# Optimization experiments

Measured on AMD Instinct MI355X. Metric: run time of the kernel, lower is better.

## Reference

```python
import jax, jax.numpy as jnp
import numpy as np

H = 8            # heads
M = 256          # num_landmarks
PINV_ITERS = 6
PAD = 16         # residual_conv_kernel(33)//2


def layernorm(x, g, b, eps=1e-5):
    mu = x.mean(-1, keepdims=True)
    var = ((x - mu) ** 2).mean(-1, keepdims=True)
    return (x - mu) * jax.lax.rsqrt(var + eps) * g + b


def moore_penrose_pinv(x, iters=PINV_ITERS):
    # iterative Moore-Penrose pseudo-inverse (Nystromformer)
    abs_x = jnp.abs(x)
    col = abs_x.sum(-1)
    row = abs_x.sum(-2)
    z = jnp.swapaxes(x, -1, -2) / (jnp.max(col) * jnp.max(row))
    eye = jnp.eye(x.shape[-1], dtype=x.dtype)
    for _ in range(iters):
        xz = x @ z
        z = 0.25 * z @ (13.0 * eye - xz @ (15.0 * eye - xz @ (7.0 * eye - xz)))
    return z


def attn_block(y, ln1_g, ln1_b, w_qkv, w_out, b_out, res_w,
               ln2_g, ln2_b, w1, b1, w2, b2):
    B, N, D = y.shape
    inner = w_qkv.shape[1] // 3
    dh = inner // H
    xn = layernorm(y, ln1_g, ln1_b)
    qkv = xn @ w_qkv                      # [B,N,3*inner]
    q, k, v = jnp.split(qkv, 3, axis=-1)
    to_heads = lambda t: t.reshape(B, N, H, dh).transpose(0, 2, 1, 3)  # [B,H,N,dh]
    q, k, v = map(to_heads, (q, k, v))
    q = q * (dh ** -0.5)
    l = N // M                            # tokens per landmark (N % M == 0 here)
    q_l = q.reshape(B, H, M, l, dh).mean(3)  # sum/l == mean -> [B,H,M,dh]
    k_l = k.reshape(B, H, M, l, dh).mean(3)
    attn1 = jax.nn.softmax(jnp.einsum('bhnd,bhmd->bhnm', q, k_l), axis=-1)
    attn2 = jax.nn.softmax(jnp.einsum('bhid,bhjd->bhij', q_l, k_l), axis=-1)
    attn3 = jax.nn.softmax(jnp.einsum('bhmd,bhnd->bhmn', q_l, k), axis=-1)
    attn2_inv = moore_penrose_pinv(attn2)
    out = (attn1 @ attn2_inv) @ (attn3 @ v)   # [B,H,N,dh]
    # depthwise residual conv over sequence dim: v as NCHW with C=H, Hdim=N, Wdim=dh
    res = jax.lax.conv_general_dilated(
        v, res_w, window_strides=(1, 1), padding=[(PAD, PAD), (0, 0)],
        dimension_numbers=('NCHW', 'OIHW', 'NCHW'), feature_group_count=H)
    out = out + res
    out = out.transpose(0, 2, 1, 3).reshape(B, N, inner)
    y = y + out @ w_out + b_out
    yn = layernorm(y, ln2_g, ln2_b)
    hdn = jax.nn.gelu(yn @ w1 + b1, approximate=False)
    return y + hdn @ w2 + b2


def setup_inputs() -> dict:
    key = jax.random.key(0)
    ks = jax.random.split(key, 8)
    B, N, D, NB = 4, 4096, 256, 2
    inner = D
    p = lambda k, shp: jax.random.normal(k, shp, jnp.float32) * 0.02
    return {
        'x': jax.random.normal(ks[0], (B, N, D), jnp.float32),
        'ln1_g': jnp.ones((NB, D), jnp.float32),
        'ln1_b': jnp.zeros((NB, D), jnp.float32),
        'w_qkv': p(ks[1], (NB, D, 3 * inner)),
        'w_out': p(ks[2], (NB, inner, D)),
        'b_out': jnp.zeros((NB, D), jnp.float32),
        'res_w': p(ks[3], (NB, H, 1, 33, 1)),
        'ln2_g': jnp.ones((NB, D), jnp.float32),
        'ln2_b': jnp.zeros((NB, D), jnp.float32),
        'w1': p(ks[4], (NB, D, 2 * D)),
        'b1': jnp.zeros((NB, 2 * D), jnp.float32),
        'w2': p(ks[5], (NB, 2 * D, D)),
        'b2': jnp.zeros((NB, D), jnp.float32),
    }


def reference(x, ln1_g, ln1_b, w_qkv, w_out, b_out, res_w,
              ln2_g, ln2_b, w1, b1, w2, b2):
    y = x
    for i in range(ln1_g.shape[0]):
        y = attn_block(y, ln1_g[i], ln1_b[i], w_qkv[i], w_out[i], b_out[i],
                       res_w[i], ln2_g[i], ln2_b[i], w1[i], b1[i], w2[i], b2[i])
    return y
```

## Files before the change

### kernel.cpp

```cpp
#include <hip/hip_runtime.h>
#include <math.h>

typedef float f32x4 __attribute__((ext_vector_type(4)));
typedef short s16x8 __attribute__((ext_vector_type(8)));
typedef unsigned short u16;
typedef unsigned int u32;

#define MFMA16(a,b,c) __builtin_amdgcn_mfma_f32_16x16x32_bf16((a),(b),(c),0,0,0)
#define AS1 __attribute__((address_space(1)))
#define AS3 __attribute__((address_space(3)))

__device__ __forceinline__ void dma16(const u16* g, u16* l){
  __builtin_amdgcn_global_load_lds((const AS1 u32*)g, (AS3 u32*)l, 16, 0, 0);
}

__device__ __forceinline__ float bf2f(u16 u){
  union { unsigned int i; float f; } v; v.i = ((unsigned int)u)<<16; return v.f;
}
__device__ __forceinline__ u16 f2bf(float f){
  union { float f; unsigned int i; } v; v.f = f;
  unsigned int x = v.i;
  return (u16)((x + 0x7fffu + ((x>>16)&1u))>>16);
}

enum { EPI_QKV=0, EPI_BIAS_GELU=3 };

template<int EPI>
__global__ __launch_bounds__(256)
void kgemm2(const u16* __restrict__ A, const u16* __restrict__ BT, int K, int lda, int ldb,
            const float* __restrict__ bias, u16* __restrict__ outb, int ldc,
            u16* __restrict__ qo, u16* __restrict__ ko, u16* __restrict__ vo,
            u16* __restrict__ qlm, u16* __restrict__ klm)
{
  __shared__ __align__(16) u16 As[128*32];
  __shared__ __align__(16) u16 Bs[128*32];
  const int tid = threadIdx.x;
  const int w = tid>>6, wy = w>>1, wx = w&1, l = tid&63, q = l>>4, ln = l&15;
  const int m0 = blockIdx.x*128, n0 = blockIdx.y*128;
  const int lrow = l>>2, lch = l&3;

  f32x4 acc[4][4];
  #pragma unroll
  for (int i=0;i<4;i++)
    #pragma unroll
    for (int j=0;j<4;j++){ acc[i][j][0]=0.f; acc[i][j][1]=0.f; acc[i][j][2]=0.f; acc[i][j][3]=0.f; }

  for (int k0=0; k0<K; k0+=32){
    #pragma unroll
    for (int c=0;c<2;c++){
      int row = 32*w + 16*c + lrow;
      int gch = lch ^ ((row>>1)&3);
      dma16(A + (long)(m0+row)*lda + k0 + gch*8, &As[(32*w+16*c)*32]);
      dma16(BT + (long)(n0+row)*ldb + k0 + gch*8, &Bs[(32*w+16*c)*32]);
    }
    __syncthreads();
    s16x8 af[4], bfr[4];
    #pragma unroll
    for (int mt=0;mt<4;mt++){
      int row = wy*64 + mt*16 + ln;
      af[mt] = *(const s16x8*)&As[row*32 + ((q ^ ((row>>1)&3))<<3)];
    }
    #pragma unroll
    for (int nt=0;nt<4;nt++){
      int row = wx*64 + nt*16 + ln;
      bfr[nt] = *(const s16x8*)&Bs[row*32 + ((q ^ ((row>>1)&3))<<3)];
    }
    #pragma unroll
    for (int mt=0;mt<4;mt++)
      #pragma unroll
      for (int nt=0;nt<4;nt++)
        acc[mt][nt] = MFMA16(af[mt], bfr[nt], acc[mt][nt]);
    __syncthreads();
  }

  #pragma unroll
  for (int mt=0;mt<4;mt++)
  #pragma unroll
  for (int nt=0;nt<4;nt++){
    int ncol = n0 + wx*64 + nt*16 + ln;
    if (EPI==EPI_QKV){
      int sel = ncol>>8, hd = ncol&255, h = hd>>5, d = hd&31;
      u16* dst = sel==0 ? qo : (sel==1 ? ko : vo);
      float sc2 = (sel==0) ? 0.17677669529663689f : 1.f;
      float s = 0.f;
      #pragma unroll
      for (int r=0;r<4;r++){
        int mrow = m0 + wy*64 + mt*16 + q*4 + r;
        int b = mrow>>12, n = mrow&4095;
        float v = acc[mt][nt][r]*sc2;
        dst[(((long)(b*8+h)*4096 + n)<<5) + d] = f2bf(v);
        s += v;
      }
      if (sel < 2){
        s += __shfl_xor(s, 16);
        s += __shfl_xor(s, 32);
        if (q == 0){
          int mrow0 = m0 + wy*64 + mt*16;
          int b = mrow0>>12, grp = (mrow0&4095)>>4;
          u16* ldst = (sel==0) ? qlm : klm;
          ldst[(((long)(b*8+h)*256 + grp)<<5) + d] = f2bf(s*(1.0f/16.0f));
        }
      }
    } else {
      #pragma unroll
      for (int r=0;r<4;r++){
        int mrow = m0 + wy*64 + mt*16 + q*4 + r;
        float x = acc[mt][nt][r] + bias[ncol];
        float g = 0.5f*x*(1.0f + erff(x*0.70710678118654752f));
        outb[(long)mrow*ldc + ncol] = f2bf(g);
      }
    }
  }
}

__global__ __launch_bounds__(256)
void kgemmLN(const u16* __restrict__ A, const u16* __restrict__ BT, int K,
             const float* __restrict__ bias, const float* __restrict__ base,
             float* __restrict__ yout,
             const float* __restrict__ lng, const float* __restrict__ lnb,
             u16* __restrict__ xnout)
{
  __shared__ __align__(16) u16 As[128*32];
  __shared__ __align__(16) u16 Bs[256*32];
  const int tid = threadIdx.x;
  const int w = tid>>6, l = tid&63, q = l>>4, ln = l&15;
  const int m0 = blockIdx.x*128;
  const int lrow = l>>2, lch = l&3;

  f32x4 acc[2][16];
  #pragma unroll
  for (int i=0;i<2;i++)
    #pragma unroll
    for (int j=0;j<16;j++){ acc[i][j][0]=0.f; acc[i][j][1]=0.f; acc[i][j][2]=0.f; acc[i][j][3]=0.f; }

  for (int k0=0; k0<K; k0+=32){
    #pragma unroll
    for (int c=0;c<2;c++){
      int row = 32*w + 16*c + lrow;
      int gch = lch ^ ((row>>1)&3);
      dma16(A + (long)(m0+row)*K + k0 + gch*8, &As[(32*w+16*c)*32]);
    }
    #pragma unroll
    for (int c=0;c<4;c++){
      int row = 64*w + 16*c + lrow;
      int gch = lch ^ ((row>>1)&3);
      dma16(BT + (long)row*K + k0 + gch*8, &Bs[(64*w+16*c)*32]);
    }
    __syncthreads();
    s16x8 af[2];
    #pragma unroll
    for (int mt=0;mt<2;mt++){
      int row = w*32 + mt*16 + ln;
      af[mt] = *(const s16x8*)&As[row*32 + ((q ^ ((row>>1)&3))<<3)];
    }
    #pragma unroll
    for (int nt=0;nt<16;nt++){
      int row = nt*16 + ln;
      s16x8 bfr = *(const s16x8*)&Bs[row*32 + ((q ^ ((row>>1)&3))<<3)];
      acc[0][nt] = MFMA16(af[0], bfr, acc[0][nt]);
      acc[1][nt] = MFMA16(af[1], bfr, acc[1][nt]);
    }
    __syncthreads();
  }

  float rb[16];
  #pragma unroll
  for (int nt=0;nt<16;nt++) rb[nt] = bias[nt*16 + ln];
  #pragma unroll
  for (int mt=0;mt<2;mt++)
  #pragma unroll
  for (int r=0;r<4;r++){
    long rowb = (long)(m0 + w*32 + mt*16 + q*4 + r)*256;
    #pragma unroll
    for (int nt=0;nt<16;nt++){
      int col = nt*16 + ln;
      float v = base[rowb + col] + acc[mt][nt][r] + rb[nt];
      acc[mt][nt][r] = v;
      yout[rowb + col] = v;
    }
  }
  float mu[2][4], rs[2][4];
  #pragma unroll
  for (int mt=0;mt<2;mt++)
  #pragma unroll
  for (int r=0;r<4;r++){
    float s = 0.f;
    #pragma unroll
    for (int nt=0;nt<16;nt++) s += acc[mt][nt][r];
    s += __shfl_xor(s,1); s += __shfl_xor(s,2); s += __shfl_xor(s,4); s += __shfl_xor(s,8);
    mu[mt][r] = s*(1.0f/256.0f);
  }
  #pragma unroll
  for (int mt=0;mt<2;mt++)
  #pragma unroll
  for (int r=0;r<4;r++){
    float vs = 0.f;
    #pragma unroll
    for (int nt=0;nt<16;nt++){ float d = acc[mt][nt][r]-mu[mt][r]; vs += d*d; }
    vs += __shfl_xor(vs,1); vs += __shfl_xor(vs,2); vs += __shfl_xor(vs,4); vs += __shfl_xor(vs,8);
    rs[mt][r] = rsqrtf(vs*(1.0f/256.0f) + 1e-5f);
  }
  float rg[16], rbb[16];
  #pragma unroll
  for (int nt=0;nt<16;nt++){ int col = nt*16+ln; rg[nt]=lng[col]; rbb[nt]=lnb[col]; }
  #pragma unroll
  for (int mt=0;mt<2;mt++)
  #pragma unroll
  for (int r=0;r<4;r++){
    long rowb = (long)(m0 + w*32 + mt*16 + q*4 + r)*256;
    #pragma unroll
    for (int nt=0;nt<16;nt++){
      int col = nt*16 + ln;
      float d = acc[mt][nt][r]-mu[mt][r];
      xnout[rowb + col] = f2bf(d*rs[mt][r]*rg[nt] + rbb[nt]);
    }
  }
}

__device__ __forceinline__ int swidx(int row, int col){
  int cc = col>>3;
  int sl = (cc&24)|((cc&7)^((row>>1)&7));
  return row*256 + sl*8 + (col&7);
}

__device__ __forceinline__ void stage256(const u16* __restrict__ g, u16* lds, int w, int l){
  const int drow = l>>5, dch = l&31;
  #pragma unroll
  for (int c=0;c<16;c++){
    int base = (c*8 + w)*2;
    int row = base + drow;
    int gch = (dch&24) | ((dch&7) ^ ((row>>1)&7));
    dma16(g + (long)row*256 + gch*8, &lds[base*256]);
  }
}

__device__ __forceinline__ void stage32(const u16* __restrict__ g, u16* lds, int w, int l){
  const int drow = l>>5, dch = l&31;
  #pragma unroll
  for (int c=0;c<2;c++){
    int base = (c*8 + w)*2;
    int row = base + drow;
    int gch = (dch&24) | ((dch&7) ^ ((row>>1)&7));
    dma16(g + (long)row*256 + gch*8, &lds[base*256]);
  }
}

__device__ __forceinline__ void mult32(const u16* aL, int arow0, const u16* bL,
                                       int w, int l, f32x4 (&acc)[2][2]){
  const int q=l>>4, ln=l&15, wn0=w*32;
  #pragma unroll
  for (int mt=0;mt<2;mt++)
    #pragma unroll
    for (int nt=0;nt<2;nt++){ acc[mt][nt][0]=0.f; acc[mt][nt][1]=0.f; acc[mt][nt][2]=0.f; acc[mt][nt][3]=0.f; }
  #pragma unroll
  for (int kq=0;kq<8;kq++){
    int ca = kq*4+q;
    s16x8 af[2];
    #pragma unroll
    for (int mt=0;mt<2;mt++){
      int r = arow0 + mt*16 + ln;
      af[mt] = *(const s16x8*)&aL[r*256 + (((ca&24)|((ca&7)^((r>>1)&7)))<<3)];
    }
    #pragma unroll
    for (int nt=0;nt<2;nt++){
      int n = wn0 + nt*16 + ln;
      s16x8 bfr = *(const s16x8*)&bL[n*256 + (((ca&24)|((ca&7)^((n>>1)&7)))<<3)];
      acc[0][nt] = MFMA16(af[0], bfr, acc[0][nt]);
      acc[1][nt] = MFMA16(af[1], bfr, acc[1][nt]);
    }
  }
}

__device__ __forceinline__ void polyinit13(const u16* aL, int arow0, int w, int l, f32x4 (&poly)[2][2]){
  const int q=l>>4, ln=l&15, wn0=w*32;
  #pragma unroll
  for (int mt=0;mt<2;mt++)
  #pragma unroll
  for (int nt=0;nt<2;nt++)
  #pragma unroll
  for (int r=0;r<4;r++){
    int row = arow0 + mt*16 + q*4 + r;
    int col = wn0 + nt*16 + ln;
    poly[mt][nt][r] = 13.f*bf2f(aL[swidx(row,col)]);
  }
}

__device__ __forceinline__ void polyaxpy(f32x4 (&poly)[2][2], const f32x4 (&acc)[2][2], float sc){
  #pragma unroll
  for (int mt=0;mt<2;mt++)
    #pragma unroll
    for (int nt=0;nt<2;nt++)
      #pragma unroll
      for (int r=0;r<4;r++) poly[mt][nt][r] += sc*acc[mt][nt][r];
}

__device__ __forceinline__ void writeT(u16* Ts, const f32x4 (&acc)[2][2], int w, int l, float sc){
  const int q=l>>4, ln=l&15, wn0=w*32;
  #pragma unroll
  for (int mt=0;mt<2;mt++)
  #pragma unroll
  for (int nt=0;nt<2;nt++)
  #pragma unroll
  for (int r=0;r<4;r++){
    int row = mt*16 + q*4 + r;
    int col = wn0 + nt*16 + ln;
    Ts[swidx(row,col)] = f2bf(sc*acc[mt][nt][r]);
  }
}

__device__ __forceinline__ void epi_poly(u16* __restrict__ out, int rowbase,
                                         const f32x4 (&poly)[2][2], int w, int l, float sc){
  const int q=l>>4, ln=l&15, wn0=w*32;
  #pragma unroll
  for (int mt=0;mt<2;mt++)
  #pragma unroll
  for (int nt=0;nt<2;nt++)
  #pragma unroll
  for (int r=0;r<4;r++){
    int row = rowbase + mt*16 + q*4 + r;
    int col = wn0 + nt*16 + ln;
    out[(long)row*256 + col] = f2bf(sc*poly[mt][nt][r]);
  }
}

__global__ __launch_bounds__(512)
void kw0(const float* __restrict__ cs_p, float* __restrict__ scal,
         const float* __restrict__ num_p, const float* __restrict__ den_p,
         const u16* __restrict__ X, u16* __restrict__ W0, u16* __restrict__ h0)
{
  __shared__ __align__(16) u16 Wf[65536];
  __shared__ __align__(16) u16 Ts[8192];
  const int tid=threadIdx.x, w=tid>>6, l=tid&63;
  const int bid=blockIdx.x, xcd=bid&7, j=bid>>3;
  const int batch = xcd*4 + (j>>3), slab = j&7;

  stage256(X + (long)batch*65536, Wf, w, l);

  float* red = (float*)Ts;
  float mx = 0.f;
  for (int i=tid;i<8192;i+=512){
    float s = 0.f;
    #pragma unroll
    for (int c=0;c<8;c++) s += cs_p[(long)c*8192 + i];
    mx = fmaxf(mx, s);
  }
  red[tid] = mx; __syncthreads();
  for (int s=256;s>0;s>>=1){ if (tid<s) red[tid] = fmaxf(red[tid], red[tid+s]); __syncthreads(); }
  float s0 = 1.0f/red[0];
  if (bid==0 && tid==0) scal[0] = s0;

  f32x4 acc[2][2];
  mult32(Wf, slab*32, Wf, w, l, acc);
  {
    const int q=l>>4, ln=l&15, wn0=w*32;
    u16* ob = W0 + (long)batch*65536;
    #pragma unroll
    for (int mt=0;mt<2;mt++)
    #pragma unroll
    for (int nt=0;nt<2;nt++)
    #pragma unroll
    for (int r=0;r<4;r++){
      int row = slab*32 + mt*16 + q*4 + r;
      int col = wn0 + nt*16 + ln;
      ob[(long)row*256 + col] = f2bf(acc[mt][nt][r]*s0);
    }
  }

  if (slab==0){
    __syncthreads();
    float (*lt)[257] = (float(*)[257])Wf;
    for (int i=tid;i<8192;i+=512){
      int m = i>>5, d = i&31;
      float sn = 0.f, sd = 0.f;
      #pragma unroll
      for (int c=0;c<8;c++){
        sn += num_p[((long)(c*32+batch))*8192 + i];
        sd += den_p[(c*32+batch)*256 + m];
      }
      lt[d][m] = sn/sd;
    }
    __syncthreads();
    u16* o = h0 + (long)batch*8192;
    for (int j2=tid;j2<8192;j2+=512){
      int d = j2>>8, m = j2&255;
      o[j2] = f2bf(lt[d][m]);
    }
  }
}

__global__ __launch_bounds__(512)
void kiter(const u16* __restrict__ Win, u16* __restrict__ Wout,
           const u16* __restrict__ hin, u16* __restrict__ hout)
{
  __shared__ __align__(16) u16 Wf[65536];
  __shared__ __align__(16) u16 Ts[8192];
  const int tid=threadIdx.x, w=tid>>6, l=tid&63;
  const int bid=blockIdx.x, xcd=bid&7, j=bid>>3;
  const int batch = xcd*4 + (j>>3), slab = j&7;

  stage256(Win + (long)batch*65536, Wf, w, l);
  __syncthreads();

  f32x4 acc[2][2], poly[2][2];
  polyinit13(Wf, slab*32, w, l, poly);
  mult32(Wf, slab*32, Wf, w, l, acc);
  polyaxpy(poly, acc, -15.f);
  writeT(Ts, acc, w, l, 1.f);
  __syncthreads();
  mult32(Ts, 0, Wf, w, l, acc);
  polyaxpy(poly, acc, 7.f);
  __syncthreads();
  writeT(Ts, acc, w, l, 1.f);
  __syncthreads();
  mult32(Ts, 0, Wf, w, l, acc);
  polyaxpy(poly, acc, -1.f);
  epi_poly(Wout + (long)batch*65536, slab*32, poly, w, l, 0.25f);

  if (slab==0){
    __syncthreads();
    stage32(hin + (long)batch*8192, Ts, w, l);
    __syncthreads();
    polyinit13(Ts, 0, w, l, poly);
    mult32(Ts, 0, Wf, w, l, acc);
    polyaxpy(poly, acc, -15.f);
    __syncthreads(); writeT(Ts, acc, w, l, 1.f); __syncthreads();
    mult32(Ts, 0, Wf, w, l, acc);
    polyaxpy(poly, acc, 7.f);
    __syncthreads(); writeT(Ts, acc, w, l, 1.f); __syncthreads();
    mult32(Ts, 0, Wf, w, l, acc);
    polyaxpy(poly, acc, -1.f);
    epi_poly(hout + (long)batch*8192, 0, poly, w, l, 0.25f);
  }
}

__global__ __launch_bounds__(512)
void ktail(const u16* __restrict__ W5, const u16* __restrict__ h5,
           const u16* __restrict__ XT, const float* __restrict__ scal,
           u16* __restrict__ uT)
{
  __shared__ __align__(16) u16 Wf[65536];
  __shared__ __align__(16) u16 Ts[8192];
  const int tid=threadIdx.x, w=tid>>6, l=tid&63;
  const int batch = blockIdx.x;

  stage256(W5 + (long)batch*65536, Wf, w, l);
  stage32(h5 + (long)batch*8192, Ts, w, l);
  __syncthreads();

  f32x4 acc[2][2], poly[2][2];
  polyinit13(Ts, 0, w, l, poly);
  mult32(Ts, 0, Wf, w, l, acc);
  polyaxpy(poly, acc, -15.f);
  __syncthreads(); writeT(Ts, acc, w, l, 1.f); __syncthreads();
  mult32(Ts, 0, Wf, w, l, acc);
  polyaxpy(poly, acc, 7.f);
  __syncthreads(); writeT(Ts, acc, w, l, 1.f); __syncthreads();
  mult32(Ts, 0, Wf, w, l, acc);
  polyaxpy(poly, acc, -1.f);
  __syncthreads();
  writeT(Ts, poly, w, l, 0.25f);
  __syncthreads();
  stage256(XT + (long)batch*65536, Wf, w, l);
  __syncthreads();
  mult32(Ts, 0, Wf, w, l, acc);
  const float s0 = scal[0];
  {
    const int q=l>>4, ln=l&15, wn0=w*32;
    u16* ob = uT + (long)batch*8192;
    #pragma unroll
    for (int mt=0;mt<2;mt++)
    #pragma unroll
    for (int nt=0;nt<2;nt++)
    #pragma unroll
    for (int r=0;r<4;r++){
      int row = mt*16 + q*4 + r;
      int col = wn0 + nt*16 + ln;
      ob[(long)row*256 + col] = f2bf(acc[mt][nt][r]*s0);
    }
  }
}

__global__ __launch_bounds__(256)
void kattn23(const u16* __restrict__ ql, const u16* __restrict__ kl,
             u16* __restrict__ X, u16* __restrict__ XT, float* __restrict__ cs_p,
             const u16* __restrict__ kk, const u16* __restrict__ vv,
             float* __restrict__ num_p, float* __restrict__ den_p)
{
  __shared__ __align__(16) u16 Pbuf[4][64][40];
  __shared__ __align__(16) u16 vT[32][40];
  __shared__ float qrow[32][33];
  __shared__ float psum[32][4];
  __shared__ float rsum[32];
  int bh = blockIdx.y;
  int tid = threadIdx.x, w = tid>>6, l = tid&63, q = l>>4, ln = l&15;

  if (blockIdx.x < 8){
    int r0 = blockIdx.x*32;
    int c = tid;
    #pragma unroll
    for (int i=0;i<4;i++){
      int e = c*4+i; int rr = e>>5, dd = e&31;
      qrow[rr][dd] = bf2f(ql[((long)bh*256 + r0+rr)*32 + dd]);
    }
    float kc[32];
    {
      const u16* kp = kl + ((long)bh*256 + c)*32;
      #pragma unroll
      for (int d=0;d<32;d++) kc[d] = bf2f(kp[d]);
    }
    __syncthreads();
    float er[32]; float colacc = 0.f;
    for (int r=0;r<32;r++){
      float s = 0.f;
      #pragma unroll
      for (int d=0;d<32;d++) s += qrow[r][d]*kc[d];
      float e = __expf(s);
      er[r] = e;
      float wsum = e;
      #pragma unroll
      for (int m=1;m<64;m<<=1) wsum += __shfl_xor(wsum, m);
      if (l==0) psum[r][w] = wsum;
    }
    __syncthreads();
    if (c<32) rsum[c] = psum[c][0]+psum[c][1]+psum[c][2]+psum[c][3];
    __syncthreads();
    for (int r=0;r<32;r++){
      float x = er[r]/rsum[r];
      u16 xb = f2bf(x);
      X [((long)bh*256 + r0+r)*256 + c] = xb;
      XT[((long)bh*256 + c)*256 + r0+r] = xb;
      colacc += x;
    }
    cs_p[(long)blockIdx.x*8192 + bh*256 + c] = colacc;
    return;
  }

  int chunk = blockIdx.x - 8;
  f32x4 z4; z4[0]=0.f; z4[1]=0.f; z4[2]=0.f; z4[3]=0.f;
  f32x4 acc[4][2]; f32x4 dacc[4];
  #pragma unroll
  for (int mt=0;mt<4;mt++){ dacc[mt]=z4; acc[mt][0]=z4; acc[mt][1]=z4; }
  const u16* qlb = ql + (long)bh*8192;
  const u16* kb  = kk + (long)bh*131072;
  const u16* vb  = vv + (long)bh*131072;
  int vn = tid>>3, vd = (tid&7)*4;
  for (int s=0;s<16;s++){
    int n0 = chunk*512 + s*32;
    ushort4 vx = *(const ushort4*)(vb + (long)(n0+vn)*32 + vd);
    vT[vd+0][vn]=vx.x; vT[vd+1][vn]=vx.y; vT[vd+2][vn]=vx.z; vT[vd+3][vn]=vx.w;
    __syncthreads();
    s16x8 bk[2];
    #pragma unroll
    for (int nt=0;nt<2;nt++) bk[nt] = *(const s16x8*)(kb + (long)(n0 + nt*16 + ln)*32 + q*8);
    #pragma unroll
    for (int mt=0;mt<4;mt++){
      s16x8 aq = *(const s16x8*)(qlb + (long)(w*64 + mt*16 + ln)*32 + q*8);
      #pragma unroll
      for (int nt=0;nt<2;nt++){
        f32x4 sf = MFMA16(aq, bk[nt], z4);
        f32x4 ef;
        #pragma unroll
        for (int r=0;r<4;r++) ef[r] = __expf(sf[r]);
        dacc[mt] += ef;
        #pragma unroll
        for (int r=0;r<4;r++) Pbuf[w][mt*16 + q*4 + r][nt*16 + ln] = f2bf(ef[r]);
      }
    }
    #pragma unroll
    for (int mt=0;mt<4;mt++){
      s16x8 ap = *(const s16x8*)&Pbuf[w][mt*16 + ln][q*8];
      #pragma unroll
      for (int nt=0;nt<2;nt++){
        s16x8 bv = *(const s16x8*)&vT[nt*16 + ln][q*8];
        acc[mt][nt] = MFMA16(ap, bv, acc[mt][nt]);
      }
    }
    __syncthreads();
  }
  #pragma unroll
  for (int mt=0;mt<4;mt++)
    #pragma unroll
    for (int r=0;r<4;r++){
      float x = dacc[mt][r];
      x += __shfl_xor(x,1); x += __shfl_xor(x,2); x += __shfl_xor(x,4); x += __shfl_xor(x,8);
      dacc[mt][r] = x;
    }
  long pbase = (long)(chunk*32 + bh);
  #pragma unroll
  for (int mt=0;mt<4;mt++)
    #pragma unroll
    for (int nt=0;nt<2;nt++)
      #pragma unroll
      for (int r=0;r<4;r++){
        int mg = w*64 + mt*16 + q*4 + r;
        num_p[pbase*8192 + (long)mg*32 + nt*16 + ln] = acc[mt][nt][r];
      }
  if (ln==0){
    #pragma unroll
    for (int mt=0;mt<4;mt++)
      #pragma unroll
      for (int r=0;r<4;r++)
        den_p[pbase*256 + w*64 + mt*16 + q*4 + r] = dacc[mt][r];
  }
}

__global__ __launch_bounds__(256)
void kattn1u(const u16* __restrict__ qq, const u16* __restrict__ kl, const u16* __restrict__ uT,
             const u16* __restrict__ vv, const float* __restrict__ rw,
             u16* __restrict__ aoutb)
{
  int nch = blockIdx.x, bh = blockIdx.y;
  int b = bh>>3, h = bh&7;
  int tid = threadIdx.x, w = tid>>6, l = tid&63, q = l>>4, ln = l&15;
  __shared__ __align__(16) u16 Pbuf[4][32][40];
  __shared__ __align__(16) u16 vtile[160][36];
  int r0g = nch*128;
  const u16* vb = vv + (long)bh*131072;
  #pragma unroll
  for (int it=0; it<5; it++){
    int slot = tid + it*256;
    int rr = slot>>3, c = (slot&7)*4;
    int s = r0g - 16 + rr;
    ushort4 val; val.x=0; val.y=0; val.z=0; val.w=0;
    if (s>=0 && s<4096) val = *(const ushort4*)(vb + (long)s*32 + c);
    *(ushort4*)&vtile[rr][c] = val;
  }
  __syncthreads();

  f32x4 z4; z4[0]=0.f; z4[1]=0.f; z4[2]=0.f; z4[3]=0.f;
  f32x4 acc[2][2]; f32x4 dacc[2];
  #pragma unroll
  for (int mt=0;mt<2;mt++){ dacc[mt]=z4; acc[mt][0]=z4; acc[mt][1]=z4; }
  const u16* qb  = qq + (long)bh*131072;
  const u16* klb = kl + (long)bh*8192;
  const u16* ub  = uT + (long)bh*8192;
  int r0 = r0g + w*32;
  for (int s=0;s<8;s++){
    s16x8 bk[2];
    #pragma unroll
    for (int nt=0;nt<2;nt++) bk[nt] = *(const s16x8*)(klb + (long)(s*32 + nt*16 + ln)*32 + q*8);
    #pragma unroll
    for (int mt=0;mt<2;mt++){
      s16x8 aq = *(const s16x8*)(qb + (long)(r0 + mt*16 + ln)*32 + q*8);
      #pragma unroll
      for (int nt=0;nt<2;nt++){
        f32x4 sf = MFMA16(aq, bk[nt], z4);
        f32x4 ef;
        #pragma unroll
        for (int r=0;r<4;r++) ef[r] = __expf(sf[r]);
        dacc[mt] += ef;
        #pragma unroll
        for (int r=0;r<4;r++) Pbuf[w][mt*16 + q*4 + r][nt*16 + ln] = f2bf(ef[r]);
      }
    }
    #pragma unroll
    for (int mt=0;mt<2;mt++){
      s16x8 ap = *(const s16x8*)&Pbuf[w][mt*16 + ln][q*8];
      #pragma unroll
      for (int nt=0;nt<2;nt++){
        s16x8 bu = *(const s16x8*)(ub + (long)(nt*16 + ln)*256 + s*32 + q*8);
        acc[mt][nt] = MFMA16(ap, bu, acc[mt][nt]);
      }
    }
  }
  #pragma unroll
  for (int mt=0;mt<2;mt++)
    #pragma unroll
    for (int r=0;r<4;r++){
      float x = dacc[mt][r];
      x += __shfl_xor(x,1); x += __shfl_xor(x,2); x += __shfl_xor(x,4); x += __shfl_xor(x,8);
      dacc[mt][r] = x;
    }

  const float* wp = rw + h*33;
  float w_[33];
  #pragma unroll
  for (int j=0;j<33;j++) w_[j] = wp[j];

  #pragma unroll
  for (int mt=0;mt<2;mt++){
    int nl = w*32 + mt*16 + q*4;
    #pragma unroll
    for (int nt=0;nt<2;nt++){
      int d = nt*16 + ln;
      float vvv[36];
      #pragma unroll
      for (int j=0;j<36;j++) vvv[j] = bf2f(vtile[nl + j][d]);
      #pragma unroll
      for (int r=0;r<4;r++){
        float cv = 0.f;
        #pragma unroll
        for (int j=0;j<33;j++) cv += w_[j]*vvv[r+j];
        int n = r0 + mt*16 + q*4 + r;
        long oidx = ((long)b*4096 + n)*256 + h*32 + d;
        aoutb[oidx] = f2bf(acc[mt][nt][r]/dacc[mt][r] + cv);
      }
    }
  }
}

__global__ __launch_bounds__(256)
void kcvtln(const float* __restrict__ xin, const float* __restrict__ lg, const float* __restrict__ lb,
            u16* __restrict__ xn,
            const float* __restrict__ wqkv, const float* __restrict__ wout,
            const float* __restrict__ w1, const float* __restrict__ w2,
            u16* __restrict__ wqkvT, u16* __restrict__ woutT,
            u16* __restrict__ w1T, u16* __restrict__ w2T)
{
  __shared__ float t[32][33];
  int z = blockIdx.x;
  if (z < 4096){
    int w = threadIdx.x>>6, l = threadIdx.x&63;
    long row = (long)z*4 + w;
    float4 v = ((const float4*)(xin + row*256))[l];
    float s = v.x+v.y+v.z+v.w;
    #pragma unroll
    for (int m=1;m<64;m<<=1) s += __shfl_xor(s, m);
    float mu = s*(1.0f/256.0f);
    float dx=v.x-mu, dy=v.y-mu, dz=v.z-mu, dw=v.w-mu;
    float s2 = dx*dx+dy*dy+dz*dz+dw*dw;
    #pragma unroll
    for (int m=1;m<64;m<<=1) s2 += __shfl_xor(s2, m);
    float rs = rsqrtf(s2*(1.0f/256.0f) + 1e-5f);
    float4 gg = ((const float4*)lg)[l];
    float4 bb = ((const float4*)lb)[l];
    ushort4 o;
    o.x = f2bf(dx*rs*gg.x + bb.x);
    o.y = f2bf(dy*rs*gg.y + bb.y);
    o.z = f2bf(dz*rs*gg.z + bb.z);
    o.w = f2bf(dw*rs*gg.w + bb.w);
    *(ushort4*)(xn + row*256 + l*4) = o;
    return;
  }
  z -= 4096;
  const float* src; u16* dst; int K, Nn, bx, by;
  if (z < 384){      int i=z/192, r=z%192; src=wqkv+(long)i*196608; dst=wqkvT+(long)i*196608; K=256; Nn=768; bx=r%24; by=r/24; }
  else if (z < 512){ int zz=z-384; int i=zz/64, r=zz%64; src=wout+(long)i*65536; dst=woutT+(long)i*65536; K=256; Nn=256; bx=r%8; by=r/8; }
  else if (z < 768){ int zz=z-512; int i=zz/128, r=zz%128; src=w1+(long)i*131072; dst=w1T+(long)i*131072; K=256; Nn=512; bx=r%16; by=r/16; }
  else {             int zz=z-768; int i=zz/128, r=zz%128; src=w2+(long)i*131072; dst=w2T+(long)i*131072; K=512; Nn=256; bx=r%8; by=r/8; }
  int n0 = bx*32, k0 = by*32;
  int tx = threadIdx.x&31, ty = threadIdx.x>>5;
  #pragma unroll
  for (int i=0;i<4;i++) t[ty+i*8][tx] = src[(long)(k0+ty+i*8)*Nn + n0+tx];
  __syncthreads();
  #pragma unroll
  for (int i=0;i<4;i++) dst[(long)(n0+ty+i*8)*K + k0+tx] = f2bf(t[tx][ty+i*8]);
}

extern "C" void kernel_launch(void* const* d_in, const int* in_sizes, int n_in,
                              void* d_out, int out_size, void* d_ws, size_t ws_size,
                              hipStream_t stream)
{
  const float* x    = (const float*)d_in[0];
  const float* ln1g = (const float*)d_in[1];
  const float* ln1b = (const float*)d_in[2];
  const float* wqkv = (const float*)d_in[3];
  const float* wout = (const float*)d_in[4];
  const float* bout = (const float*)d_in[5];
  const float* resw = (const float*)d_in[6];
  const float* ln2g = (const float*)d_in[7];
  const float* ln2b = (const float*)d_in[8];
  const float* w1   = (const float*)d_in[9];
  const float* b1   = (const float*)d_in[10];
  const float* w2   = (const float*)d_in[11];
  const float* b2   = (const float*)d_in[12];
  float* y = (float*)d_out;
  char* ws = (char*)d_ws;

  u16* xn    = (u16*)(ws + 0);
  u16* qb    = (u16*)(ws + 8388608);
  u16* kb    = (u16*)(ws + 16777216);
  u16* vb    = (u16*)(ws + 25165824);
  u16* ql    = (u16*)(ws + 33554432);
  u16* kl    = (u16*)(ws + 34078720);
  u16* X     = (u16*)(ws + 34603008);
  u16* XT    = (u16*)(ws + 38797312);
  u16* h0b   = (u16*)(ws + 42991616);
  u16* WA    = (u16*)(ws + 51380224);
  u16* WB    = (u16*)(ws + 55574528);
  u16* hA    = (u16*)(ws + 68157440);
  u16* hB    = (u16*)(ws + 72351744);
  float* num_p = (float*)(ws + 76546048);
  float* den_p = (float*)(ws + 84934656);
  float* cs_p  = (float*)(ws + 85196800);
  float* scal  = (float*)(ws + 85458944);
  u16* uT    = (u16*)(ws + 85459200);
  u16* aoutb = (u16*)(ws + 85983488);
  u16* wqkvT = (u16*)(ws + 94372096);
  u16* woutT = (u16*)(ws + 95158528);
  u16* w1T   = (u16*)(ws + 95420672);
  u16* w2T   = (u16*)(ws + 95944960);
  u16* hdn   = (u16*)(ws + 51380224);

  (void)in_sizes; (void)n_in; (void)out_size; (void)ws_size;

  kcvtln<<<5120,256,0,stream>>>(x, ln1g, ln1b, xn,
      wqkv, wout, w1, w2, wqkvT, woutT, w1T, w2T);

  for (int i=0;i<2;i++){
    kgemm2<EPI_QKV><<<dim3(128,6),256,0,stream>>>(xn, wqkvT + (long)i*196608, 256, 256, 256,
        nullptr, nullptr, 0, qb,kb,vb, ql,kl);
    kattn23<<<dim3(16,32),256,0,stream>>>(ql, kl, X, XT, cs_p, kb, vb, num_p, den_p);

    kw0<<<256,512,0,stream>>>(cs_p, scal, num_p, den_p, X, WA, h0b);
    u16 *Wi = WA, *Wo = WB, *hi = h0b, *ho = hA;
    for (int it=0; it<5; it++){
      kiter<<<256,512,0,stream>>>(Wi, Wo, hi, ho);
      u16* t = Wi; Wi = Wo; Wo = t;
      hi = ho; ho = (ho == hA) ? hB : hA;
    }
    ktail<<<32,512,0,stream>>>(Wi, hi, XT, scal, uT);

    kattn1u<<<dim3(32,32),256,0,stream>>>(qb, kl, uT, vb, resw + i*264, aoutb);
    kgemmLN<<<128,256,0,stream>>>(aoutb, woutT + (long)i*65536, 256,
        bout + i*256, i==0 ? x : y, y, ln2g + i*256, ln2b + i*256, xn);
    kgemm2<EPI_BIAS_GELU><<<dim3(128,4),256,0,stream>>>(xn, w1T + (long)i*131072, 256, 256, 256,
        b1 + i*512, hdn, 512, nullptr,nullptr,nullptr, nullptr,nullptr);
    kgemmLN<<<128,256,0,stream>>>(hdn, w2T + (long)i*131072, 512,
        b2 + i*256, y, y, ln1g + 256, ln1b + 256, xn);
  }
}
```

Before: 536.7 us.

## Spread h-iteration across slabs, cache B fragments in registers, shrink LN-GEMM tiles

```diff
diff --git a/kernel.cpp b/kernel.cpp
--- a/kernel.cpp
+++ b/kernel.cpp
@@ -120,99 +120,111 @@
              const float* __restrict__ lng, const float* __restrict__ lnb,
              u16* __restrict__ xnout)
 {
-  __shared__ __align__(16) u16 As[128*32];
+  __shared__ __align__(16) u16 As[64*32];
   __shared__ __align__(16) u16 Bs[256*32];
+  __shared__ float red[64][4];
   const int tid = threadIdx.x;
   const int w = tid>>6, l = tid&63, q = l>>4, ln = l&15;
-  const int m0 = blockIdx.x*128;
-  const int lrow = l>>2, lch = l&3;
-
-  f32x4 acc[2][16];
-  #pragma unroll
-  for (int i=0;i<2;i++)
-    #pragma unroll
-    for (int j=0;j<16;j++){ acc[i][j][0]=0.f; acc[i][j][1]=0.f; acc[i][j][2]=0.f; acc[i][j][3]=0.f; }
+  const int m0 = blockIdx.x*64;
+
+  f32x4 acc[4][4];
+  #pragma unroll
+  for (int i=0;i<4;i++)
+    #pragma unroll
+    for (int j=0;j<4;j++){ acc[i][j][0]=0.f; acc[i][j][1]=0.f; acc[i][j][2]=0.f; acc[i][j][3]=0.f; }
 
   for (int k0=0; k0<K; k0+=32){
-    #pragma unroll
-    for (int c=0;c<2;c++){
-      int row = 32*w + 16*c + lrow;
-      int gch = lch ^ ((row>>1)&3);
-      dma16(A + (long)(m0+row)*K + k0 + gch*8, &As[(32*w+16*c)*32]);
+    {
+      int row = w*16 + (l>>2);
+      int gch = (l&3) ^ ((row>>1)&3);
+      dma16(A + (long)(m0+row)*K + k0 + gch*8, &As[(w*16)*32]);
     }
     #pragma unroll
     for (int c=0;c<4;c++){
-      int row = 64*w + 16*c + lrow;
-      int gch = lch ^ ((row>>1)&3);
-      dma16(BT + (long)row*K + k0 + gch*8, &Bs[(64*w+16*c)*32]);
-    }
-    __syncthreads();
-    s16x8 af[2];
-    #pragma unroll
-    for (int mt=0;mt<2;mt++){
-      int row = w*32 + mt*16 + ln;
+      int row = c*64 + w*16 + (l>>2);
+      int gch = (l&3) ^ ((row>>1)&3);
+      dma16(BT + (long)row*K + k0 + gch*8, &Bs[(c*64+w*16)*32]);
+    }
+    __syncthreads();
+    s16x8 af[4], bfr[4];
+    #pragma unroll
+    for (int mt=0;mt<4;mt++){
+      int row = mt*16 + ln;
       af[mt] = *(const s16x8*)&As[row*32 + ((q ^ ((row>>1)&3))<<3)];
     }
     #pragma unroll
-    for (int nt=0;nt<16;nt++){
-      int row = nt*16 + ln;
-      s16x8 bfr = *(const s16x8*)&Bs[row*32 + ((q ^ ((row>>1)&3))<<3)];
-      acc[0][nt] = MFMA16(af[0], bfr, acc[0][nt]);
-      acc[1][nt] = MFMA16(af[1], bfr, acc[1][nt]);
-    }
-    __syncthreads();
-  }
-
-  float rb[16];
-  #pragma unroll
-  for (int nt=0;nt<16;nt++) rb[nt] = bias[nt*16 + ln];
-  #pragma unroll
-  for (int mt=0;mt<2;mt++)
+    for (int nt=0;nt<4;nt++){
+      int row = w*64 + nt*16 + ln;
+      bfr[nt] = *(const s16x8*)&Bs[row*32 + ((q ^ ((row>>1)&3))<<3)];
+    }
+    #pragma unroll
+    for (int mt=0;mt<4;mt++)
+      #pragma unroll
+      for (int nt=0;nt<4;nt++)
+        acc[mt][nt] = MFMA16(af[mt], bfr[nt], acc[mt][nt]);
+    __syncthreads();
+  }
+
+  float rb[4];
+  #pragma unroll
+  for (int nt=0;nt<4;nt++) rb[nt] = bias[w*64 + nt*16 + ln];
+  #pragma unroll
+  for (int mt=0;mt<4;mt++)
   #pragma unroll
   for (int r=0;r<4;r++){
-    long rowb = (long)(m0 + w*32 + mt*16 + q*4 + r)*256;
-    #pragma unroll
-    for (int nt=0;nt<16;nt++){
-      int col = nt*16 + ln;
+    long rowb = (long)(m0 + mt*16 + q*4 + r)*256;
+    #pragma unroll
+    for (int nt=0;nt<4;nt++){
+      int col = w*64 + nt*16 + ln;
       float v = base[rowb + col] + acc[mt][nt][r] + rb[nt];
       acc[mt][nt][r] = v;
       yout[rowb + col] = v;
     }
   }
-  float mu[2][4], rs[2][4];
-  #pragma unroll
-  for (int mt=0;mt<2;mt++)
+  #pragma unroll
+  for (int mt=0;mt<4;mt++)
   #pragma unroll
   for (int r=0;r<4;r++){
-    float s = 0.f;
-    #pragma unroll
-    for (int nt=0;nt<16;nt++) s += acc[mt][nt][r];
+    float s = acc[mt][0][r]+acc[mt][1][r]+acc[mt][2][r]+acc[mt][3][r];
     s += __shfl_xor(s,1); s += __shfl_xor(s,2); s += __shfl_xor(s,4); s += __shfl_xor(s,8);
-    mu[mt][r] = s*(1.0f/256.0f);
-  }
-  #pragma unroll
-  for (int mt=0;mt<2;mt++)
+    if (ln==0) red[mt*16+q*4+r][w] = s;
+  }
+  __syncthreads();
+  float mu[4][4];
+  #pragma unroll
+  for (int mt=0;mt<4;mt++)
+  #pragma unroll
+  for (int r=0;r<4;r++){
+    int row = mt*16+q*4+r;
+    mu[mt][r] = (red[row][0]+red[row][1]+red[row][2]+red[row][3])*(1.0f/256.0f);
+  }
+  __syncthreads();
+  #pragma unroll
+  for (int mt=0;mt<4;mt++)
   #pragma unroll
   for (int r=0;r<4;r++){
     float vs = 0.f;
     #pragma unroll
-    for (int nt=0;nt<16;nt++){ float d = acc[mt][nt][r]-mu[mt][r]; vs += d*d; }
+    for (int nt=0;nt<4;nt++){ float d = acc[mt][nt][r]-mu[mt][r]; vs += d*d; }
     vs += __shfl_xor(vs,1); vs += __shfl_xor(vs,2); vs += __shfl_xor(vs,4); vs += __shfl_xor(vs,8);
-    rs[mt][r] = rsqrtf(vs*(1.0f/256.0f) + 1e-5f);
-  }
-  float rg[16], rbb[16];
-  #pragma unroll
-  for (int nt=0;nt<16;nt++){ int col = nt*16+ln; rg[nt]=lng[col]; rbb[nt]=lnb[col]; }
-  #pragma unroll
-  for (int mt=0;mt<2;mt++)
+    if (ln==0) red[mt*16+q*4+r][w] = vs;
+  }
+  __syncthreads();
+  float rg[4], rbb[4];
+  #pragma unroll
+  for (int nt=0;nt<4;nt++){ int col = w*64+nt*16+ln; rg[nt]=lng[col]; rbb[nt]=lnb[col]; }
+  #pragma unroll
+  for (int mt=0;mt<4;mt++)
   #pragma unroll
   for (int r=0;r<4;r++){
-    long rowb = (long)(m0 + w*32 + mt*16 + q*4 + r)*256;
-    #pragma unroll
-    for (int nt=0;nt<16;nt++){
-      int col = nt*16 + ln;
+    int row = mt*16+q*4+r;
+    float rs = rsqrtf((red[row][0]+red[row][1]+red[row][2]+red[row][3])*(1.0f/256.0f) + 1e-5f);
+    long rowb = (long)(m0 + row)*256;
+    #pragma unroll
+    for (int nt=0;nt<4;nt++){
+      int col = w*64 + nt*16 + ln;
       float d = acc[mt][nt][r]-mu[mt][r];
-      xnout[rowb + col] = f2bf(d*rs[mt][r]*rg[nt] + rbb[nt]);
+      xnout[rowb + col] = f2bf(d*rs*rg[nt] + rbb[nt]);
     }
   }
 }
@@ -221,6 +233,9 @@
   int cc = col>>3;
   int sl = (cc&24)|((cc&7)^((row>>1)&7));
   return row*256 + sl*8 + (col&7);
+}
+__device__ __forceinline__ int slot8(int ca, int row){
+  return ((ca&24)|((ca&7)^((row>>1)&7)))<<3;
 }
 
 __device__ __forceinline__ void stage256(const u16* __restrict__ g, u16* lds, int w, int l){
@@ -233,7 +248,6 @@
     dma16(g + (long)row*256 + gch*8, &lds[base*256]);
   }
 }
-
 __device__ __forceinline__ void stage32(const u16* __restrict__ g, u16* lds, int w, int l){
   const int drow = l>>5, dch = l&31;
   #pragma unroll
@@ -244,10 +258,27 @@
     dma16(g + (long)row*256 + gch*8, &lds[base*256]);
   }
 }
-
-__device__ __forceinline__ void mult32(const u16* aL, int arow0, const u16* bL,
-                                       int w, int l, f32x4 (&acc)[2][2]){
+__device__ __forceinline__ void stage16(const u16* __restrict__ g, u16* lds, int w, int l){
+  const int drow = l>>5, dch = l&31;
+  int row = w*2 + drow;
+  int gch = (dch&24) | ((dch&7) ^ ((row>>1)&7));
+  dma16(g + (long)row*256 + gch*8, &lds[(w*2)*256]);
+}
+
+__device__ __forceinline__ void loadBf(const u16* bL, int w, int l, s16x8 (&bw)[2][8]){
   const int q=l>>4, ln=l&15, wn0=w*32;
+  #pragma unroll
+  for (int nt=0;nt<2;nt++)
+    #pragma unroll
+    for (int kq=0;kq<8;kq++){
+      int n = wn0 + nt*16 + ln, ca = kq*4+q;
+      bw[nt][kq] = *(const s16x8*)&bL[n*256 + slot8(ca, n)];
+    }
+}
+
+__device__ __forceinline__ void multAr(const u16* aL, int arow0, const s16x8 (&bw)[2][8],
+                                       int l, f32x4 (&acc)[2][2]){
+  const int q=l>>4, ln=l&15;
   #pragma unroll
   for (int mt=0;mt<2;mt++)
     #pragma unroll
@@ -259,15 +290,27 @@
     #pragma unroll
     for (int mt=0;mt<2;mt++){
       int r = arow0 + mt*16 + ln;
-      af[mt] = *(const s16x8*)&aL[r*256 + (((ca&24)|((ca&7)^((r>>1)&7)))<<3)];
-    }
-    #pragma unroll
-    for (int nt=0;nt<2;nt++){
-      int n = wn0 + nt*16 + ln;
-      s16x8 bfr = *(const s16x8*)&bL[n*256 + (((ca&24)|((ca&7)^((n>>1)&7)))<<3)];
-      acc[0][nt] = MFMA16(af[0], bfr, acc[0][nt]);
-      acc[1][nt] = MFMA16(af[1], bfr, acc[1][nt]);
-    }
+      af[mt] = *(const s16x8*)&aL[r*256 + slot8(ca, r)];
+    }
+    #pragma unroll
+    for (int mt=0;mt<2;mt++)
+      #pragma unroll
+      for (int nt=0;nt<2;nt++)
+        acc[mt][nt] = MFMA16(af[mt], bw[nt][kq], acc[mt][nt]);
+  }
+}
+
+__device__ __forceinline__ void multHr(const u16* hL, const s16x8 (&bw)[2][8],
+                                       int l, f32x4 (&hacc)[2]){
+  const int q=l>>4, ln=l&15;
+  hacc[0][0]=0.f; hacc[0][1]=0.f; hacc[0][2]=0.f; hacc[0][3]=0.f;
+  hacc[1][0]=0.f; hacc[1][1]=0.f; hacc[1][2]=0.f; hacc[1][3]=0.f;
+  #pragma unroll
+  for (int kq=0;kq<8;kq++){
+    int ca = kq*4+q;
+    s16x8 af = *(const s16x8*)&hL[ln*256 + slot8(ca, ln)];
+    hacc[0] = MFMA16(af, bw[0][kq], hacc[0]);
+    hacc[1] = MFMA16(af, bw[1][kq], hacc[1]);
   }
 }
 
@@ -284,7 +327,14 @@
     poly[mt][nt][r] = 13.f*bf2f(aL[swidx(row,col)]);
   }
 }
-
+__device__ __forceinline__ void init13H(const u16* hL, int w, int l, f32x4 (&hpoly)[2]){
+  const int q=l>>4, ln=l&15, wn0=w*32;
+  #pragma unroll
+  for (int nt=0;nt<2;nt++)
+  #pragma unroll
+  for (int r=0;r<4;r++)
+    hpoly[nt][r] = 13.f*bf2f(hL[swidx(q*4+r, wn0+nt*16+ln)]);
+}
 __device__ __forceinline__ void polyaxpy(f32x4 (&poly)[2][2], const f32x4 (&acc)[2][2], float sc){
   #pragma unroll
   for (int mt=0;mt<2;mt++)
@@ -293,7 +343,12 @@
       #pragma unroll
       for (int r=0;r<4;r++) poly[mt][nt][r] += sc*acc[mt][nt][r];
 }
-
+__device__ __forceinline__ void axpyH(f32x4 (&hpoly)[2], const f32x4 (&hacc)[2], float sc){
+  #pragma unroll
+  for (int nt=0;nt<2;nt++)
+    #pragma unroll
+    for (int r=0;r<4;r++) hpoly[nt][r] += sc*hacc[nt][r];
+}
 __device__ __forceinline__ void writeT(u16* Ts, const f32x4 (&acc)[2][2], int w, int l, float sc){
   const int q=l>>4, ln=l&15, wn0=w*32;
   #pragma unroll
@@ -307,7 +362,14 @@
     Ts[swidx(row,col)] = f2bf(sc*acc[mt][nt][r]);
   }
 }
-
+__device__ __forceinline__ void writeH(u16* Hs, const f32x4 (&hacc)[2], int w, int l){
+  const int q=l>>4, ln=l&15, wn0=w*32;
+  #pragma unroll
+  for (int nt=0;nt<2;nt++)
+  #pragma unroll
+  for (int r=0;r<4;r++)
+    Hs[swidx(q*4+r, wn0+nt*16+ln)] = f2bf(hacc[nt][r]);
+}
 __device__ __forceinline__ void epi_poly(u16* __restrict__ out, int rowbase,
                                          const f32x4 (&poly)[2][2], int w, int l, float sc){
   const int q=l>>4, ln=l&15, wn0=w*32;
@@ -320,6 +382,41 @@
     int row = rowbase + mt*16 + q*4 + r;
     int col = wn0 + nt*16 + ln;
     out[(long)row*256 + col] = f2bf(sc*poly[mt][nt][r]);
+  }
+}
+__device__ __forceinline__ void epiH(u16* __restrict__ out, const f32x4 (&hpoly)[2],
+                                     int w, int l, float sc){
+  const int q=l>>4, ln=l&15, wn0=w*32;
+  #pragma unroll
+  for (int nt=0;nt<2;nt++)
+  #pragma unroll
+  for (int r=0;r<4;r++)
+    out[(long)(q*4+r)*256 + wn0+nt*16+ln] = f2bf(sc*hpoly[nt][r]);
+}
+
+__device__ __forceinline__ void mult32(const u16* aL, int arow0, const u16* bL,
+                                       int w, int l, f32x4 (&acc)[2][2]){
+  const int q=l>>4, ln=l&15, wn0=w*32;
+  #pragma unroll
+  for (int mt=0;mt<2;mt++)
+    #pragma unroll
+    for (int nt=0;nt<2;nt++){ acc[mt][nt][0]=0.f; acc[mt][nt][1]=0.f; acc[mt][nt][2]=0.f; acc[mt][nt][3]=0.f; }
+  #pragma unroll
+  for (int kq=0;kq<8;kq++){
+    int ca = kq*4+q;
+    s16x8 af[2];
+    #pragma unroll
+    for (int mt=0;mt<2;mt++){
+      int r = arow0 + mt*16 + ln;
+      af[mt] = *(const s16x8*)&aL[r*256 + slot8(ca,r)];
+    }
+    #pragma unroll
+    for (int nt=0;nt<2;nt++){
+      int n = wn0 + nt*16 + ln;
+      s16x8 bfr = *(const s16x8*)&bL[n*256 + slot8(ca,n)];
+      acc[0][nt] = MFMA16(af[0], bfr, acc[0][nt]);
+      acc[1][nt] = MFMA16(af[1], bfr, acc[1][nt]);
+    }
   }
 }
 
@@ -394,42 +491,49 @@
 {
   __shared__ __align__(16) u16 Wf[65536];
   __shared__ __align__(16) u16 Ts[8192];
+  __shared__ __align__(16) u16 Hs[4096];
   const int tid=threadIdx.x, w=tid>>6, l=tid&63;
   const int bid=blockIdx.x, xcd=bid&7, j=bid>>3;
   const int batch = xcd*4 + (j>>3), slab = j&7;
+  const bool hrole = (slab&3)==0;
+  const int hr0 = (slab>>2)*16;
 
   stage256(Win + (long)batch*65536, Wf, w, l);
-  __syncthreads();
+  if (hrole) stage16(hin + (long)batch*8192 + hr0*256, Hs, w, l);
+  __syncthreads();
+
+  s16x8 bw[2][8];
+  loadBf(Wf, w, l, bw);
 
   f32x4 acc[2][2], poly[2][2];
+  f32x4 hacc[2], hpoly[2];
+
   polyinit13(Wf, slab*32, w, l, poly);
-  mult32(Wf, slab*32, Wf, w, l, acc);
+  multAr(Wf, slab*32, bw, l, acc);
   polyaxpy(poly, acc, -15.f);
+  if (hrole){
+    init13H(Hs, w, l, hpoly);
+    multHr(Hs, bw, l, hacc);
+    axpyH(hpoly, hacc, -15.f);
+  }
+  __syncthreads();
   writeT(Ts, acc, w, l, 1.f);
-  __syncthreads();
-  mult32(Ts, 0, Wf, w, l, acc);
+  if (hrole) writeH(Hs, hacc, w, l);
+  __syncthreads();
+  multAr(Ts, 0, bw, l, acc);
   polyaxpy(poly, acc, 7.f);
+  if (hrole){ multHr(Hs, bw, l, hacc); axpyH(hpoly, hacc, 7.f); }
   __syncthreads();
   writeT(Ts, acc, w, l, 1.f);
-  __syncthreads();
-  mult32(Ts, 0, Wf, w, l, acc);
+  if (hrole) writeH(Hs, hacc, w, l);
+  __syncthreads();
+  multAr(Ts, 0, bw, l, acc);
   polyaxpy(poly, acc, -1.f);
   epi_poly(Wout + (long)batch*65536, slab*32, poly, w, l, 0.25f);
-
-  if (slab==0){
-    __syncthreads();
-    stage32(hin + (long)batch*8192, Ts, w, l);
-    __syncthreads();
-    polyinit13(Ts, 0, w, l, poly);
-    mult32(Ts, 0, Wf, w, l, acc);
-    polyaxpy(poly, acc, -15.f);
-    __syncthreads(); writeT(Ts, acc, w, l, 1.f); __syncthreads();
-    mult32(Ts, 0, Wf, w, l, acc);
-    polyaxpy(poly, acc, 7.f);
-    __syncthreads(); writeT(Ts, acc, w, l, 1.f); __syncthreads();
-    mult32(Ts, 0, Wf, w, l, acc);
-    polyaxpy(poly, acc, -1.f);
-    epi_poly(hout + (long)batch*8192, 0, poly, w, l, 0.25f);
+  if (hrole){
+    multHr(Hs, bw, l, hacc);
+    axpyH(hpoly, hacc, -1.f);
+    epiH(hout + (long)batch*8192 + hr0*256, hpoly, w, l, 0.25f);
   }
 }
 
@@ -447,22 +551,25 @@
   stage32(h5 + (long)batch*8192, Ts, w, l);
   __syncthreads();
 
+  s16x8 bw[2][8];
+  loadBf(Wf, w, l, bw);
+
   f32x4 acc[2][2], poly[2][2];
   polyinit13(Ts, 0, w, l, poly);
-  mult32(Ts, 0, Wf, w, l, acc);
+  multAr(Ts, 0, bw, l, acc);
   polyaxpy(poly, acc, -15.f);
   __syncthreads(); writeT(Ts, acc, w, l, 1.f); __syncthreads();
-  mult32(Ts, 0, Wf, w, l, acc);
+  multAr(Ts, 0, bw, l, acc);
   polyaxpy(poly, acc, 7.f);
   __syncthreads(); writeT(Ts, acc, w, l, 1.f); __syncthreads();
-  mult32(Ts, 0, Wf, w, l, acc);
+  multAr(Ts, 0, bw, l, acc);
   polyaxpy(poly, acc, -1.f);
   __syncthreads();
   writeT(Ts, poly, w, l, 0.25f);
-  __syncthreads();
   stage256(XT + (long)batch*65536, Wf, w, l);
   __syncthreads();
-  mult32(Ts, 0, Wf, w, l, acc);
+  loadBf(Wf, w, l, bw);
+  multAr(Ts, 0, bw, l, acc);
   const float s0 = scal[0];
   {
     const int q=l>>4, ln=l&15, wn0=w*32;
@@ -812,11 +919,11 @@
     ktail<<<32,512,0,stream>>>(Wi, hi, XT, scal, uT);
 
     kattn1u<<<dim3(32,32),256,0,stream>>>(qb, kl, uT, vb, resw + i*264, aoutb);
-    kgemmLN<<<128,256,0,stream>>>(aoutb, woutT + (long)i*65536, 256,
+    kgemmLN<<<256,256,0,stream>>>(aoutb, woutT + (long)i*65536, 256,
         bout + i*256, i==0 ? x : y, y, ln2g + i*256, ln2b + i*256, xn);
     kgemm2<EPI_BIAS_GELU><<<dim3(128,4),256,0,stream>>>(xn, w1T + (long)i*131072, 256, 256, 256,
         b1 + i*512, hdn, 512, nullptr,nullptr,nullptr, nullptr,nullptr);
-    kgemmLN<<<128,256,0,stream>>>(hdn, w2T + (long)i*131072, 512,
+    kgemmLN<<<256,256,0,stream>>>(hdn, w2T + (long)i*131072, 512,
         b2 + i*256, y, y, ln1g + 256, ln1b + 256, xn);
   }
 }
```

After: 501.6 us, median of 2. 1.07x faster.
